# Optimization experiments

Hardware: AMD Instinct MI355X
Metric: run time of the kernel (lower is better)

## Reference

```python
import jax, jax.numpy as jnp
from jax import lax
import numpy as np

WINDOW = 8
ENCOLEN = 128
HID = 128
INT_H = 128


def setup_inputs() -> dict:
    key = jax.random.key(0)
    ks = jax.random.split(key, 16)
    s = 0.05
    B, T = 512, 256
    return {
        "input_X": jax.random.normal(ks[0], (B, T, 7), jnp.float32),
        "W_ih": jax.random.normal(ks[1], (4 * HID, 5), jnp.float32) * s,
        "W_hh": jax.random.normal(ks[2], (4 * HID, HID), jnp.float32) * s,
        "b_ih": jax.random.normal(ks[3], (4 * HID,), jnp.float32) * s,
        "b_hh": jax.random.normal(ks[4], (4 * HID,), jnp.float32) * s,
        "fc1_w": jax.random.normal(ks[5], (HID, HID), jnp.float32) * s,
        "fc1_b": jax.random.normal(ks[6], (HID,), jnp.float32) * s,
        "fc2_w": jax.random.normal(ks[7], (1, HID), jnp.float32) * s,
        "fc2_b": jax.random.normal(ks[8], (1,), jnp.float32) * s,
        "int1_w": jax.random.normal(ks[9], (INT_H, 3), jnp.float32) * s,
        "int1_b": jax.random.normal(ks[10], (INT_H,), jnp.float32) * s,
        "int3_w": jax.random.normal(ks[11], (1, INT_H), jnp.float32) * s,
        "int3_b": jax.random.normal(ks[12], (1,), jnp.float32) * s,
        "scale_w": jax.random.normal(ks[13], (1, 1), jnp.float32) * s,
        "zone_w": jax.random.normal(ks[14], (1, 1), jnp.float32) * s,
    }


def _forward(input_X, W_ih, W_hh, b_ih, b_hh, fc1_w, fc1_b, fc2_w, fc2_b,
             int1_w, int1_b, int3_w, int3_b, scale_w, zone_w):
    B, T, _ = input_X.shape
    w = WINDOW
    T0 = input_X[:, :, 0:1]      # zone temperature
    Ext_X = input_X[:, :, 1:5]   # cols [1,2,3,4]
    Int_X = input_X[:, :, 3:6]   # cols [3,4,5]
    HVAC_X = input_X[:, :, 6:7]  # col [6]

    def lstm_chunk(h, c, xs):  # xs: [B, w, 5]
        def step(carry, x_t):
            h, c = carry
            g = x_t @ W_ih.T + b_ih + h @ W_hh.T + b_hh
            gi, gf, gg, go = jnp.split(g, 4, axis=-1)  # torch gate order i,f,g,o
            c = jax.nn.sigmoid(gf) * c + jax.nn.sigmoid(gi) * jnp.tanh(gg)
            h = jax.nn.sigmoid(go) * jnp.tanh(c)
            return (h, c), None
        (h, c), _ = lax.scan(step, (h, c), jnp.swapaxes(xs, 0, 1))
        return h, c  # final h == lstm_out[:, -1, :]

    def ext_module(h, c, xs):
        h, c = lstm_chunk(h, c, xs)
        o = jax.nn.relu(h @ fc1_w.T + fc1_b)
        return o @ fc2_w.T + fc2_b, h, c  # [B,1]

    # internal module is pointwise per timestep -> vectorize over all T
    # (note: FC2 in the torch module is defined but unused; faithful skip)
    int_all = jax.nn.sigmoid(
        jax.nn.relu(Int_X @ int1_w.T + int1_b) @ int3_w.T + int3_b
    ) @ scale_w.T  # [B,T,1]

    TOut = jnp.zeros((B, T, 1), input_X.dtype).at[:, :w].set(T0[:, :w])
    h = jnp.ones((B, HID), input_X.dtype)
    c = jnp.ones((B, HID), input_X.dtype)
    E = T0[:, w:w + 1, :]  # [B,1,1]

    def enc_step(carry, i):
        TOut, h, c, E = carry
        ratio = i.astype(input_X.dtype) / ENCOLEN
        TOut = lax.dynamic_update_slice(TOut, E, (0, i, 0))
        s = i - w + 1
        Tin = lax.dynamic_slice(T0, (0, s, 0), (B, w, 1))
        TOsl = lax.dynamic_slice(TOut, (0, s, 0), (B, w, 1))
        Exsl = lax.dynamic_slice(Ext_X, (0, s, 0), (B, w, 4))
        embed = jnp.concatenate([Tin * ratio + TOsl * (1.0 - ratio), Exsl], axis=2)
        ext, h, c = ext_module(h, c, embed)
        hv = lax.dynamic_slice(HVAC_X, (0, i, 0), (B, 1, 1))[:, 0]
        it = lax.dynamic_slice(int_all, (0, i, 0), (B, 1, 1))[:, 0]
        total = ext + hv + it  # [B,1]
        T0i = lax.dynamic_slice(T0, (0, i, 0), (B, 1, 1))
        E = ratio * T0i + (1.0 - ratio) * E + (total @ zone_w.T)[:, None, :]
        return (TOut, h, c, E), ext

    (TOut, h, c, E), ext_enc = lax.scan(enc_step, (TOut, h, c, E), jnp.arange(w, ENCOLEN))

    def dec_step(carry, i):
        TOut, h, c, E = carry
        TOut = lax.dynamic_update_slice(TOut, E, (0, i, 0))
        s = i - w + 1
        TOsl = lax.dynamic_slice(TOut, (0, s, 0), (B, w, 1))
        Exsl = lax.dynamic_slice(Ext_X, (0, s, 0), (B, w, 4))
        embed = jnp.concatenate([TOsl, Exsl], axis=2)
        ext, h, c = ext_module(h, c, embed)
        hv = lax.dynamic_slice(HVAC_X, (0, i, 0), (B, 1, 1))[:, 0]
        it = lax.dynamic_slice(int_all, (0, i, 0), (B, 1, 1))[:, 0]
        total = ext + hv + it
        E = (total @ zone_w.T)[:, None, :] + E
        return (TOut, h, c, E), ext

    (TOut, h, c, E), ext_dec = lax.scan(dec_step, (TOut, h, c, E), jnp.arange(ENCOLEN, T))

    Ext_list = jnp.zeros((B, T, 1), input_X.dtype)
    Ext_list = Ext_list.at[:, w:ENCOLEN].set(jnp.swapaxes(ext_enc, 0, 1))
    Ext_list = Ext_list.at[:, ENCOLEN:].set(jnp.swapaxes(ext_dec, 0, 1))
    Int_list = jnp.zeros((B, T, 1), input_X.dtype).at[:, w:].set(int_all[:, w:])
    HVAC_list = HVAC_X  # torch fills HVAC_list with HVAC_X at every step
    return TOut, HVAC_list, (Ext_list, Int_list)


def reference(input_X, W_ih, W_hh, b_ih, b_hh, fc1_w, fc1_b, fc2_w, fc2_b,
              int1_w, int1_b, int3_w, int3_b, scale_w, zone_w):
    return _forward(input_X, W_ih, W_hh, b_ih, b_hh, fc1_w, fc1_b, fc2_w, fc2_b,
                    int1_w, int1_b, int3_w, int3_b, scale_w, zone_w)
```

## Files before the change

### kernel.cpp

```cpp
#include <hip/hip_runtime.h>

#define BT   (512*256)
#define HB0b 192
#define HB1b 320
#define HLENb 448
#define LOG2E 1.44269504088896f

using short8  = __attribute__((ext_vector_type(8))) short;
using floatx4 = __attribute__((ext_vector_type(4))) float;
using int4v   = __attribute__((ext_vector_type(4))) int;
using ushort4v= __attribute__((ext_vector_type(4))) unsigned short;

__device__ inline unsigned short f2bf(float f){
  unsigned int u = __float_as_uint(f);
  u += 0x7FFFu + ((u >> 16) & 1u);
  return (unsigned short)(u >> 16);
}
__device__ inline float bf2f(unsigned short u){
  return __uint_as_float(((unsigned int)u) << 16);
}
__device__ inline float rcpf(float x){ return __builtin_amdgcn_rcpf(x); }
__device__ inline float ex2(float x){ return __builtin_amdgcn_exp2f(x); }

__global__ __launch_bounds__(512,1) void k_seq(
    const float* __restrict__ in,
    const float* __restrict__ Wih,  const float* __restrict__ Whh,
    const float* __restrict__ bih,  const float* __restrict__ bhh,
    const float* __restrict__ fc1w, const float* __restrict__ fc1b,
    const float* __restrict__ fc2w, const float* __restrict__ fc2b,
    const float* __restrict__ i1w,  const float* __restrict__ i1b,
    const float* __restrict__ i3w,  const float* __restrict__ i3b,
    const float* __restrict__ scw,  const float* __restrict__ zonew,
    float* __restrict__ out)
{
  __shared__ __align__(16) signed char hbuf[2][HLENb];
  __shared__ __align__(16) float scratch[640];
  __shared__ __align__(8)  unsigned short toutl[512];
  __shared__ __align__(8)  unsigned short extl[512];
  __shared__ __align__(16) unsigned short exl[2048];
  __shared__ float t0l[512];
  __shared__ float hvitl[512];
  __shared__ __align__(16) float parts[16];

  const int tid = threadIdx.x;
  const int wv  = tid >> 6;
  const int ln  = tid & 63;
  const int l15 = ln & 15;
  const int quad= ln >> 4;
  const int bb  = blockIdx.x;

  {
    int b=tid>>8, tt=tid&255;
    const float* row = in + (2*bb+b)*1792 + tt*7;
    t0l[tid] = row[0];
    exl[tid*4+0]=f2bf(row[1]); exl[tid*4+1]=f2bf(row[2]);
    exl[tid*4+2]=f2bf(row[3]); exl[tid*4+3]=f2bf(row[4]);
  }
  for(int p=tid; p<2*HLENb; p+=512) ((signed char*)hbuf)[p]=0;
  if(tid<16) toutl[(tid>>3)*256+(tid&7)] = f2bf(in[(2*bb+(tid>>3))*1792+(tid&7)*7]);
  float* lw4 = scratch;
  float* l3  = scratch + 512;
  if(tid<128){
    lw4[tid*4+0]=i1w[tid*3+0]; lw4[tid*4+1]=i1w[tid*3+1];
    lw4[tid*4+2]=i1w[tid*3+2]; lw4[tid*4+3]=i1b[tid];
    l3[tid]=i3w[tid];
  }
  __syncthreads();
  if(tid<256) hbuf[0][((tid>>7)? HB1b:HB0b) + (tid&127)] = 127;

  {
    const float b30=i3b[0], sc0=scw[0];
    int b=tid>>8, t=tid&255;
    const float* row = in + (2*bb+b)*1792 + t*7;
    float x0=row[3],x1=row[4],x2=row[5], acc=0.f;
    #pragma unroll 8
    for(int j=0;j<128;j++){
      float r=fmaxf(lw4[j*4]*x0+lw4[j*4+1]*x1+lw4[j*4+2]*x2+lw4[j*4+3],0.f);
      acc += r*l3[j];
    }
    float v = rcpf(1.f+__expf(-(acc+b30)))*sc0;
    float itv = (t<8)?0.f:v;
    int gb = 2*bb+b;
    hvitl[tid] = row[6] + itv;
    out[3*BT+gb*256+t]=itv;
    out[BT+gb*256+t]=row[6];
    if(t<8){ out[gb*256+t]=row[0]; out[2*BT+gb*256+t]=0.f; }
  }

  int4v wq[4][2];
  float dq[4];
  short8 xfr[4];
  float  bsum[4];
  #pragma unroll
  for(int g=0;g<4;g++){
    int n = 128*g + 16*wv + l15;
    bsum[g] = (bih[n]+bhh[n])*LOG2E;
    const float* wr = Whh + n*128;
    float mx = 1e-20f;
    for(int j=0;j<128;j++) mx = fmaxf(mx, fabsf(wr[j]));
    float qs = 127.f/mx;
    dq[g] = mx * (LOG2E/16129.f);
    #pragma unroll
    for(int c=0;c<2;c++){
      int4v v4;
      #pragma unroll
      for(int d=0;d<4;d++){
        int pk=0;
        #pragma unroll
        for(int bq=0;bq<4;bq++){
          int kk = c*64 + quad*16 + d*4 + bq;
          int q = __float2int_rn(wr[kk]*qs);
          pk |= (q & 255) << (8*bq);
        }
        v4[d]=pk;
      }
      wq[g][c]=v4;
    }
    short8 f;
    #pragma unroll
    for(int j=0;j<8;j++){ int kk=quad*8+j; f[j]=(short)f2bf(kk<5?Wih[n*5+kk]*LOG2E:0.f); }
    xfr[g]=f;
  }
  int4v fq[2]; float dqf;
  {
    int n2 = 16*wv + l15;
    const float* fr = fc1w + n2*128;
    float mx = 1e-20f;
    for(int j=0;j<128;j++) mx = fmaxf(mx, fabsf(fr[j]));
    float qs = 127.f/mx;
    dqf = mx * (1.f/16129.f);
    #pragma unroll
    for(int c=0;c<2;c++){
      int4v v4;
      #pragma unroll
      for(int d=0;d<4;d++){
        int pk=0;
        #pragma unroll
        for(int bq=0;bq<4;bq++){
          int kk = c*64 + quad*16 + d*4 + bq;
          int q = __float2int_rn(fr[kk]*qs);
          pk |= (q & 255) << (8*bq);
        }
        v4[d]=pk;
      }
      fq[c]=v4;
    }
  }

  const int  u     = 16*wv + l15;
  const int  bm    = quad & 1;
  const int  arow  = ((l15&3)==0) ? (((l15>>2)&1)? HB1b : HB0b) : 0;
  const int  aoff  = arow + quad*16;
  const int  hwoff = (bm? HB1b:HB0b) + u;
  const int  bpa0  = ((quad&1)<<7) | (l15<<2);
  const int  bpa1  = bpa0 + 64;
  const float fb    = fc1b[u];
  const float fcw_u = fc2w[u];
  const float fc2b0 = fc2b[0];
  const float zwv   = zonew[0];
  const floatx4 ZV  = {0.f,0.f,0.f,0.f};
  const int4v   ZI  = {0,0,0,0};
  const short8  Z8  = 0;
  float E0 = in[(2*bb)*1792 + 56];
  float E1 = in[(2*bb+1)*1792 + 56];
  float c0 = 1.f;
  __syncthreads();

  #pragma unroll 1
  for(int i=8;i<256;i++){
    if(i>8){
      floatx4 pa=*(const floatx4*)&parts[0];
      floatx4 pb=*(const floatx4*)&parts[4];
      floatx4 pc=*(const floatx4*)&parts[8];
      floatx4 pd=*(const floatx4*)&parts[12];
      float ext0=((pa[0]+pa[1])+(pa[2]+pa[3]))+((pb[0]+pb[1])+(pb[2]+pb[3]))+fc2b0;
      float ext1=((pc[0]+pc[1])+(pc[2]+pc[3]))+((pd[0]+pd[1])+(pd[2]+pd[3]))+fc2b0;
      int ip = i-1;
      float tot0 = ext0 + hvitl[ip];
      float tot1 = ext1 + hvitl[256+ip];
      if(ip<128){
        float ratio=(float)ip*0.0078125f;
        E0 = ratio*t0l[ip]     + (1.f-ratio)*E0 + tot0*zwv;
        E1 = ratio*t0l[256+ip] + (1.f-ratio)*E1 + tot1*zwv;
      } else {
        E0 += tot0*zwv;
        E1 += tot1*zwv;
      }
      if(tid==0){ extl[ip]=f2bf(ext0); extl[256+ip]=f2bf(ext1); }
    }
    if(tid==0){ toutl[i]=f2bf(E0); toutl[256+i]=f2bf(E1); }
    float xv[8][4];
    {
      short8 ea = Z8;
      if(quad==0){
        int bE=l15>>3, kk=l15&7, p=i-7+kk;
        float tos = (p==i) ? (bE? E1:E0) : bf2f(toutl[bE*256+p]);
        float tmix;
        if(i<128){
          float ratio=(float)i*0.0078125f;
          tmix = t0l[bE*256+p]*ratio + tos*(1.f-ratio);
        } else tmix = tos;
        ea[0]=(short)f2bf(tmix);
        ushort4v e4 = *(const ushort4v*)&exl[(bE*256+p)*4];
        ea[1]=(short)e4[0]; ea[2]=(short)e4[1];
        ea[3]=(short)e4[2]; ea[4]=(short)e4[3];
      }
      #pragma unroll
      for(int g=0;g<4;g++){
        floatx4 z=__builtin_amdgcn_mfma_f32_16x16x32_bf16(ea, xfr[g], ZV,0,0,0);
        #pragma unroll
        for(int r=0;r<4;r++){
          int zi = __float_as_int(z[r]+bsum[g]);
          xv[r][g]   = __int_as_float(__builtin_amdgcn_ds_bpermute(bpa0, zi));
          xv[r+4][g] = __int_as_float(__builtin_amdgcn_ds_bpermute(bpa1, zi));
        }
      }
    }

    #pragma unroll
    for(int k=0;k<8;k++){
      const signed char* hb = &hbuf[k&1][0];
      int4v a0 = *(const int4v*)(hb + aoff);
      int4v a1 = *(const int4v*)(hb + aoff + 64);
      int4v acc[4];
      #pragma unroll
      for(int g=0;g<4;g++){
        int4v z = __builtin_amdgcn_mfma_i32_16x16x64_i8(a0, wq[g][0], ZI,0,0,0);
        z = __builtin_amdgcn_mfma_i32_16x16x64_i8(a1, wq[g][1], z,0,0,0);
        acc[g]=z;
      }
      float gi=fmaf((float)acc[0][0],dq[0],xv[k][0]);
      float gf=fmaf((float)acc[1][0],dq[1],xv[k][1]);
      float gg=fmaf((float)acc[2][0],dq[2],xv[k][2]);
      float go=fmaf((float)acc[3][0],dq[3],xv[k][3]);
      float ef =ex2(-gf);
      float egi=ex2(-gi);
      float egg=ex2(-2.f*gg);
      float sf = rcpf(1.f+ef);
      float itn=(1.f-egg)*rcpf((1.f+egi)*(1.f+egg));
      c0 = sf*c0 + itn;
      float ego=ex2(-go);
      float ec =ex2(-2.8853900818f*c0);
      float hv2=(1.f-ec)*rcpf((1.f+ego)*(1.f+ec));
      int q = __float2int_rn(hv2*127.f);
      hbuf[(k+1)&1][hwoff] = (signed char)q;
      __syncthreads();
    }

    {
      const signed char* hb = &hbuf[0][0];
      int4v a0 = *(const int4v*)(hb + aoff);
      int4v a1 = *(const int4v*)(hb + aoff + 64);
      int4v z = __builtin_amdgcn_mfma_i32_16x16x64_i8(a0, fq[0], ZI,0,0,0);
      z = __builtin_amdgcn_mfma_i32_16x16x64_i8(a1, fq[1], z,0,0,0);
      float fv = (float)z[0]*dqf + fb;
      float pv = fmaxf(fv,0.f)*fcw_u;
      pv += __shfl_xor(pv, 1, 64);
      pv += __shfl_xor(pv, 2, 64);
      pv += __shfl_xor(pv, 4, 64);
      pv += __shfl_xor(pv, 8, 64);
      if(ln==0)       parts[wv]   = pv;
      else if(ln==16) parts[8+wv] = pv;
    }
    __syncthreads();
  }

  if(tid==0){
    float ext0 = ((parts[0]+parts[1])+(parts[2]+parts[3]))
               + ((parts[4]+parts[5])+(parts[6]+parts[7])) + fc2b0;
    float ext1 = ((parts[8]+parts[9])+(parts[10]+parts[11]))
               + ((parts[12]+parts[13])+(parts[14]+parts[15])) + fc2b0;
    extl[255]=f2bf(ext0); extl[511]=f2bf(ext1);
  }
  __syncthreads();

  for(int p=tid; p<496; p+=512){
    int b = (p>=248) ? 1 : 0;
    int i2 = p - b*248 + 8;
    int gb = 2*bb + b;
    out[gb*256+i2]      = bf2f(toutl[b*256+i2]);
    out[2*BT+gb*256+i2] = bf2f(extl[b*256+i2]);
  }
}

extern "C" void kernel_launch(void* const* d_in, const int* in_sizes, int n_in,
                              void* d_out, int out_size, void* d_ws, size_t ws_size,
                              hipStream_t stream)
{
  const float* in   = (const float*)d_in[0];
  const float* Wih  = (const float*)d_in[1];
  const float* Whh  = (const float*)d_in[2];
  const float* bih  = (const float*)d_in[3];
  const float* bhh  = (const float*)d_in[4];
  const float* fc1w = (const float*)d_in[5];
  const float* fc1b = (const float*)d_in[6];
  const float* fc2w = (const float*)d_in[7];
  const float* fc2b = (const float*)d_in[8];
  const float* i1w  = (const float*)d_in[9];
  const float* i1b  = (const float*)d_in[10];
  const float* i3w  = (const float*)d_in[11];
  const float* i3b  = (const float*)d_in[12];
  const float* scw  = (const float*)d_in[13];
  const float* zw   = (const float*)d_in[14];
  float* out = (float*)d_out;

  k_seq<<<dim3(256), dim3(512), 0, stream>>>(in, Wih, Whh, bih, bhh,
                                             fc1w, fc1b, fc2w, fc2b,
                                             i1w, i1b, i3w, i3b, scw, zw, out);
}
```

Baseline: 969.3 us.

## Process one batch row per block and launch twice as many blocks

```diff
diff --git a/kernel.cpp b/kernel.cpp
--- a/kernel.cpp
+++ b/kernel.cpp
@@ -2,8 +2,7 @@
 
 #define BT   (512*256)
 #define HB0b 192
-#define HB1b 320
-#define HLENb 448
+#define HLENb 320
 #define LOG2E 1.44269504088896f
 
 using short8  = __attribute__((ext_vector_type(8))) short;
@@ -22,7 +21,7 @@
 __device__ inline float rcpf(float x){ return __builtin_amdgcn_rcpf(x); }
 __device__ inline float ex2(float x){ return __builtin_amdgcn_exp2f(x); }
 
-__global__ __launch_bounds__(512,1) void k_seq(
+__global__ __launch_bounds__(512,2) void k_seq(
     const float* __restrict__ in,
     const float* __restrict__ Wih,  const float* __restrict__ Whh,
     const float* __restrict__ bih,  const float* __restrict__ bhh,
@@ -35,12 +34,12 @@
 {
   __shared__ __align__(16) signed char hbuf[2][HLENb];
   __shared__ __align__(16) float scratch[640];
-  __shared__ __align__(8)  unsigned short toutl[512];
-  __shared__ __align__(8)  unsigned short extl[512];
-  __shared__ __align__(16) unsigned short exl[2048];
-  __shared__ float t0l[512];
-  __shared__ float hvitl[512];
-  __shared__ __align__(16) float parts[16];
+  __shared__ __align__(8)  unsigned short toutl[256];
+  __shared__ __align__(8)  unsigned short extl[256];
+  __shared__ __align__(16) unsigned short exl[1024];
+  __shared__ float t0l[256];
+  __shared__ float hvitl[256];
+  __shared__ __align__(16) float parts[8];
 
   const int tid = threadIdx.x;
   const int wv  = tid >> 6;
@@ -49,29 +48,29 @@
   const int quad= ln >> 4;
   const int bb  = blockIdx.x;
 
-  {
-    int b=tid>>8, tt=tid&255;
-    const float* row = in + (2*bb+b)*1792 + tt*7;
+  if(tid<256){
+    const float* row = in + bb*1792 + tid*7;
     t0l[tid] = row[0];
     exl[tid*4+0]=f2bf(row[1]); exl[tid*4+1]=f2bf(row[2]);
     exl[tid*4+2]=f2bf(row[3]); exl[tid*4+3]=f2bf(row[4]);
   }
   for(int p=tid; p<2*HLENb; p+=512) ((signed char*)hbuf)[p]=0;
-  if(tid<16) toutl[(tid>>3)*256+(tid&7)] = f2bf(in[(2*bb+(tid>>3))*1792+(tid&7)*7]);
+  if(tid<8) toutl[tid] = f2bf(in[bb*1792+tid*7]);
   float* lw4 = scratch;
   float* l3  = scratch + 512;
-  if(tid<128){
-    lw4[tid*4+0]=i1w[tid*3+0]; lw4[tid*4+1]=i1w[tid*3+1];
-    lw4[tid*4+2]=i1w[tid*3+2]; lw4[tid*4+3]=i1b[tid];
-    l3[tid]=i3w[tid];
+  if(tid>=256 && tid<384){
+    int j=tid-256;
+    lw4[j*4+0]=i1w[j*3+0]; lw4[j*4+1]=i1w[j*3+1];
+    lw4[j*4+2]=i1w[j*3+2]; lw4[j*4+3]=i1b[j];
+    l3[j]=i3w[j];
   }
   __syncthreads();
-  if(tid<256) hbuf[0][((tid>>7)? HB1b:HB0b) + (tid&127)] = 127;
-
-  {
+  if(tid<128) hbuf[0][HB0b+tid] = 127;
+
+  if(tid<256){
     const float b30=i3b[0], sc0=scw[0];
-    int b=tid>>8, t=tid&255;
-    const float* row = in + (2*bb+b)*1792 + t*7;
+    int t=tid;
+    const float* row = in + bb*1792 + t*7;
     float x0=row[3],x1=row[4],x2=row[5], acc=0.f;
     #pragma unroll 8
     for(int j=0;j<128;j++){
@@ -80,11 +79,10 @@
     }
     float v = rcpf(1.f+__expf(-(acc+b30)))*sc0;
     float itv = (t<8)?0.f:v;
-    int gb = 2*bb+b;
-    hvitl[tid] = row[6] + itv;
-    out[3*BT+gb*256+t]=itv;
-    out[BT+gb*256+t]=row[6];
-    if(t<8){ out[gb*256+t]=row[0]; out[2*BT+gb*256+t]=0.f; }
+    hvitl[t] = row[6] + itv;
+    out[3*BT+bb*256+t]=itv;
+    out[BT+bb*256+t]=row[6];
+    if(t<8){ out[bb*256+t]=row[0]; out[2*BT+bb*256+t]=0.f; }
   }
 
   int4v wq[4][2];
@@ -148,11 +146,10 @@
   }
 
   const int  u     = 16*wv + l15;
-  const int  bm    = quad & 1;
-  const int  arow  = ((l15&3)==0) ? (((l15>>2)&1)? HB1b : HB0b) : 0;
+  const int  arow  = ((l15&3)==0) ? HB0b : 0;
   const int  aoff  = arow + quad*16;
-  const int  hwoff = (bm? HB1b:HB0b) + u;
-  const int  bpa0  = ((quad&1)<<7) | (l15<<2);
+  const int  hwoff = HB0b + u;
+  const int  bpa0  = l15<<2;
   const int  bpa1  = bpa0 + 64;
   const float fb    = fc1b[u];
   const float fcw_u = fc2w[u];
@@ -161,8 +158,7 @@
   const floatx4 ZV  = {0.f,0.f,0.f,0.f};
   const int4v   ZI  = {0,0,0,0};
   const short8  Z8  = 0;
-  float E0 = in[(2*bb)*1792 + 56];
-  float E1 = in[(2*bb+1)*1792 + 56];
+  float E0 = in[bb*1792 + 56];
   float c0 = 1.f;
   __syncthreads();
 
@@ -171,37 +167,31 @@
     if(i>8){
       floatx4 pa=*(const floatx4*)&parts[0];
       floatx4 pb=*(const floatx4*)&parts[4];
-      floatx4 pc=*(const floatx4*)&parts[8];
-      floatx4 pd=*(const floatx4*)&parts[12];
       float ext0=((pa[0]+pa[1])+(pa[2]+pa[3]))+((pb[0]+pb[1])+(pb[2]+pb[3]))+fc2b0;
-      float ext1=((pc[0]+pc[1])+(pc[2]+pc[3]))+((pd[0]+pd[1])+(pd[2]+pd[3]))+fc2b0;
       int ip = i-1;
       float tot0 = ext0 + hvitl[ip];
-      float tot1 = ext1 + hvitl[256+ip];
       if(ip<128){
         float ratio=(float)ip*0.0078125f;
-        E0 = ratio*t0l[ip]     + (1.f-ratio)*E0 + tot0*zwv;
-        E1 = ratio*t0l[256+ip] + (1.f-ratio)*E1 + tot1*zwv;
+        E0 = ratio*t0l[ip] + (1.f-ratio)*E0 + tot0*zwv;
       } else {
         E0 += tot0*zwv;
-        E1 += tot1*zwv;
-      }
-      if(tid==0){ extl[ip]=f2bf(ext0); extl[256+ip]=f2bf(ext1); }
-    }
-    if(tid==0){ toutl[i]=f2bf(E0); toutl[256+i]=f2bf(E1); }
+      }
+      if(tid==0) extl[ip]=f2bf(ext0);
+    }
+    if(tid==0) toutl[i]=f2bf(E0);
     float xv[8][4];
     {
       short8 ea = Z8;
-      if(quad==0){
-        int bE=l15>>3, kk=l15&7, p=i-7+kk;
-        float tos = (p==i) ? (bE? E1:E0) : bf2f(toutl[bE*256+p]);
+      if(ln<8){
+        int p=i-7+ln;
+        float tos = (p==i) ? E0 : bf2f(toutl[p]);
         float tmix;
         if(i<128){
           float ratio=(float)i*0.0078125f;
-          tmix = t0l[bE*256+p]*ratio + tos*(1.f-ratio);
+          tmix = t0l[p]*ratio + tos*(1.f-ratio);
         } else tmix = tos;
         ea[0]=(short)f2bf(tmix);
-        ushort4v e4 = *(const ushort4v*)&exl[(bE*256+p)*4];
+        ushort4v e4 = *(const ushort4v*)&exl[p*4];
         ea[1]=(short)e4[0]; ea[2]=(short)e4[1];
         ea[3]=(short)e4[2]; ea[4]=(short)e4[3];
       }
@@ -259,8 +249,7 @@
       pv += __shfl_xor(pv, 2, 64);
       pv += __shfl_xor(pv, 4, 64);
       pv += __shfl_xor(pv, 8, 64);
-      if(ln==0)       parts[wv]   = pv;
-      else if(ln==16) parts[8+wv] = pv;
+      if(ln==0) parts[wv] = pv;
     }
     __syncthreads();
   }
@@ -268,18 +257,14 @@
   if(tid==0){
     float ext0 = ((parts[0]+parts[1])+(parts[2]+parts[3]))
                + ((parts[4]+parts[5])+(parts[6]+parts[7])) + fc2b0;
-    float ext1 = ((parts[8]+parts[9])+(parts[10]+parts[11]))
-               + ((parts[12]+parts[13])+(parts[14]+parts[15])) + fc2b0;
-    extl[255]=f2bf(ext0); extl[511]=f2bf(ext1);
+    extl[255]=f2bf(ext0);
   }
   __syncthreads();
 
-  for(int p=tid; p<496; p+=512){
-    int b = (p>=248) ? 1 : 0;
-    int i2 = p - b*248 + 8;
-    int gb = 2*bb + b;
-    out[gb*256+i2]      = bf2f(toutl[b*256+i2]);
-    out[2*BT+gb*256+i2] = bf2f(extl[b*256+i2]);
+  if(tid<248){
+    int i2 = tid + 8;
+    out[bb*256+i2]      = bf2f(toutl[i2]);
+    out[2*BT+bb*256+i2] = bf2f(extl[i2]);
   }
 }
 
@@ -304,7 +289,7 @@
   const float* zw   = (const float*)d_in[14];
   float* out = (float*)d_out;
 
-  k_seq<<<dim3(256), dim3(512), 0, stream>>>(in, Wih, Whh, bih, bhh,
+  k_seq<<<dim3(512), dim3(512), 0, stream>>>(in, Wih, Whh, bih, bhh,
                                              fc1w, fc1b, fc2w, fc2b,
                                              i1w, i1b, i3w, i3b, scw, zw, out);
 }
```

Result: slower. 1.774 ms (+83.1%).

## Precompute next window's input projection during current step and split MFMA accumulation chains

Applied to the files above, without the earlier changes.

```diff
diff --git a/kernel.cpp b/kernel.cpp
--- a/kernel.cpp
+++ b/kernel.cpp
@@ -91,10 +91,12 @@
   float dq[4];
   short8 xfr[4];
   float  bsum[4];
+  float  wihc[4];
   #pragma unroll
   for(int g=0;g<4;g++){
     int n = 128*g + 16*wv + l15;
     bsum[g] = (bih[n]+bhh[n])*LOG2E;
+    wihc[g] = Wih[n*5]*LOG2E;
     const float* wr = Whh + n*128;
     float mx = 1e-20f;
     for(int j=0;j<128;j++) mx = fmaxf(mx, fabsf(wr[j]));
@@ -165,6 +167,49 @@
   float E1 = in[(2*bb+1)*1792 + 56];
   float c0 = 1.f;
   __syncthreads();
+
+  float xv[8][4];
+  float xvn[8][4];
+
+  auto bulk = [&](int it, bool exact7, float (&dst)[8][4]) {
+    short8 ea = Z8;
+    if(quad==0){
+      int bE=l15>>3, kk=l15&7, p=it-7+kk;
+      bool lt = (it<128);
+      float ratio=(float)it*0.0078125f;
+      float tmix;
+      if(kk==7){
+        if(exact7){
+          float tos = bE? E1:E0;
+          tmix = lt ? t0l[bE*256+it]*ratio + tos*(1.f-ratio) : tos;
+        } else {
+          tmix = lt ? t0l[bE*256+it]*ratio : 0.f;
+        }
+      } else if(kk==6){
+        float tos = exact7 ? bf2f(toutl[bE*256+p]) : (bE? E1:E0);
+        tmix = lt ? t0l[bE*256+p]*ratio + tos*(1.f-ratio) : tos;
+      } else {
+        float tos = bf2f(toutl[bE*256+p]);
+        tmix = lt ? t0l[bE*256+p]*ratio + tos*(1.f-ratio) : tos;
+      }
+      ea[0]=(short)f2bf(tmix);
+      ushort4v e4 = *(const ushort4v*)&exl[(bE*256+p)*4];
+      ea[1]=(short)e4[0]; ea[2]=(short)e4[1];
+      ea[3]=(short)e4[2]; ea[4]=(short)e4[3];
+    }
+    #pragma unroll
+    for(int g=0;g<4;g++){
+      floatx4 z=__builtin_amdgcn_mfma_f32_16x16x32_bf16(ea, xfr[g], ZV,0,0,0);
+      #pragma unroll
+      for(int r=0;r<4;r++){
+        int zi = __float_as_int(z[r]+bsum[g]);
+        dst[r][g]   = __int_as_float(__builtin_amdgcn_ds_bpermute(bpa0, zi));
+        dst[r+4][g] = __int_as_float(__builtin_amdgcn_ds_bpermute(bpa1, zi));
+      }
+    }
+  };
+
+  bulk(8, true, xv);
 
   #pragma unroll 1
   for(int i=8;i<256;i++){
@@ -187,52 +232,39 @@
         E1 += tot1*zwv;
       }
       if(tid==0){ extl[ip]=f2bf(ext0); extl[256+ip]=f2bf(ext1); }
+      float kap = (i<128) ? (1.f-(float)i*0.0078125f) : 1.f;
+      float ce  = kap * (bm ? E1 : E0);
+      #pragma unroll
+      for(int k2=0;k2<7;k2++)
+        #pragma unroll
+        for(int g=0;g<4;g++) xv[k2][g]=xvn[k2][g];
+      #pragma unroll
+      for(int g=0;g<4;g++) xv[7][g] = fmaf(ce, wihc[g], xvn[7][g]);
     }
     if(tid==0){ toutl[i]=f2bf(E0); toutl[256+i]=f2bf(E1); }
-    float xv[8][4];
-    {
-      short8 ea = Z8;
-      if(quad==0){
-        int bE=l15>>3, kk=l15&7, p=i-7+kk;
-        float tos = (p==i) ? (bE? E1:E0) : bf2f(toutl[bE*256+p]);
-        float tmix;
-        if(i<128){
-          float ratio=(float)i*0.0078125f;
-          tmix = t0l[bE*256+p]*ratio + tos*(1.f-ratio);
-        } else tmix = tos;
-        ea[0]=(short)f2bf(tmix);
-        ushort4v e4 = *(const ushort4v*)&exl[(bE*256+p)*4];
-        ea[1]=(short)e4[0]; ea[2]=(short)e4[1];
-        ea[3]=(short)e4[2]; ea[4]=(short)e4[3];
-      }
-      #pragma unroll
-      for(int g=0;g<4;g++){
-        floatx4 z=__builtin_amdgcn_mfma_f32_16x16x32_bf16(ea, xfr[g], ZV,0,0,0);
-        #pragma unroll
-        for(int r=0;r<4;r++){
-          int zi = __float_as_int(z[r]+bsum[g]);
-          xv[r][g]   = __int_as_float(__builtin_amdgcn_ds_bpermute(bpa0, zi));
-          xv[r+4][g] = __int_as_float(__builtin_amdgcn_ds_bpermute(bpa1, zi));
-        }
-      }
-    }
+
+    int4v a0h = *(const int4v*)(&hbuf[0][0] + aoff);
+    int4v a1h = *(const int4v*)(&hbuf[0][0] + aoff + 64);
+
+    if(i<255) bulk(i+1, false, xvn);
 
     #pragma unroll
     for(int k=0;k<8;k++){
       const signed char* hb = &hbuf[k&1][0];
-      int4v a0 = *(const int4v*)(hb + aoff);
-      int4v a1 = *(const int4v*)(hb + aoff + 64);
-      int4v acc[4];
+      int4v a0, a1;
+      if(k==0){ a0=a0h; a1=a1h; }
+      else { a0 = *(const int4v*)(hb + aoff); a1 = *(const int4v*)(hb + aoff + 64); }
+      int accs[4];
       #pragma unroll
       for(int g=0;g<4;g++){
-        int4v z = __builtin_amdgcn_mfma_i32_16x16x64_i8(a0, wq[g][0], ZI,0,0,0);
-        z = __builtin_amdgcn_mfma_i32_16x16x64_i8(a1, wq[g][1], z,0,0,0);
-        acc[g]=z;
-      }
-      float gi=fmaf((float)acc[0][0],dq[0],xv[k][0]);
-      float gf=fmaf((float)acc[1][0],dq[1],xv[k][1]);
-      float gg=fmaf((float)acc[2][0],dq[2],xv[k][2]);
-      float go=fmaf((float)acc[3][0],dq[3],xv[k][3]);
+        int4v za = __builtin_amdgcn_mfma_i32_16x16x64_i8(a0, wq[g][0], ZI,0,0,0);
+        int4v zb = __builtin_amdgcn_mfma_i32_16x16x64_i8(a1, wq[g][1], ZI,0,0,0);
+        accs[g] = za[0]+zb[0];
+      }
+      float gi=fmaf((float)accs[0],dq[0],xv[k][0]);
+      float gf=fmaf((float)accs[1],dq[1],xv[k][1]);
+      float gg=fmaf((float)accs[2],dq[2],xv[k][2]);
+      float go=fmaf((float)accs[3],dq[3],xv[k][3]);
       float ef =ex2(-gf);
       float egi=ex2(-gi);
       float egg=ex2(-2.f*gg);
@@ -251,9 +283,9 @@
       const signed char* hb = &hbuf[0][0];
       int4v a0 = *(const int4v*)(hb + aoff);
       int4v a1 = *(const int4v*)(hb + aoff + 64);
-      int4v z = __builtin_amdgcn_mfma_i32_16x16x64_i8(a0, fq[0], ZI,0,0,0);
-      z = __builtin_amdgcn_mfma_i32_16x16x64_i8(a1, fq[1], z,0,0,0);
-      float fv = (float)z[0]*dqf + fb;
+      int4v za = __builtin_amdgcn_mfma_i32_16x16x64_i8(a0, fq[0], ZI,0,0,0);
+      int4v zb = __builtin_amdgcn_mfma_i32_16x16x64_i8(a1, fq[1], ZI,0,0,0);
+      float fv = (float)(za[0]+zb[0])*dqf + fb;
       float pv = fmaxf(fv,0.f)*fcw_u;
       pv += __shfl_xor(pv, 1, 64);
       pv += __shfl_xor(pv, 2, 64);
```

Result: slower. 1.109 ms (+14.4%).

## Pack input projections as bf16 pairs and break MFMA accumulate chains

Applied to the files above, without the earlier changes.

```diff
diff --git a/kernel.cpp b/kernel.cpp
--- a/kernel.cpp
+++ b/kernel.cpp
@@ -2,8 +2,8 @@
 
 #define BT   (512*256)
 #define HB0b 192
-#define HB1b 320
-#define HLENb 448
+#define HB1b 336
+#define HLENb 464
 #define LOG2E 1.44269504088896f
 
 using short8  = __attribute__((ext_vector_type(8))) short;
@@ -189,7 +189,7 @@
       if(tid==0){ extl[ip]=f2bf(ext0); extl[256+ip]=f2bf(ext1); }
     }
     if(tid==0){ toutl[i]=f2bf(E0); toutl[256+i]=f2bf(E1); }
-    float xv[8][4];
+    int xvp[8][2];
     {
       short8 ea = Z8;
       if(quad==0){
@@ -206,13 +206,17 @@
         ea[3]=(short)e4[2]; ea[4]=(short)e4[3];
       }
       #pragma unroll
-      for(int g=0;g<4;g++){
-        floatx4 z=__builtin_amdgcn_mfma_f32_16x16x32_bf16(ea, xfr[g], ZV,0,0,0);
+      for(int gp=0; gp<2; gp++){
+        floatx4 zl=__builtin_amdgcn_mfma_f32_16x16x32_bf16(ea, xfr[2*gp],   ZV,0,0,0);
+        floatx4 zh=__builtin_amdgcn_mfma_f32_16x16x32_bf16(ea, xfr[2*gp+1], ZV,0,0,0);
         #pragma unroll
         for(int r=0;r<4;r++){
-          int zi = __float_as_int(z[r]+bsum[g]);
-          xv[r][g]   = __int_as_float(__builtin_amdgcn_ds_bpermute(bpa0, zi));
-          xv[r+4][g] = __int_as_float(__builtin_amdgcn_ds_bpermute(bpa1, zi));
+          float lo = zl[r]+bsum[2*gp];
+          float hi = zh[r]+bsum[2*gp+1];
+          int pk;
+          asm("v_cvt_pk_bf16_f32 %0, %1, %2" : "=v"(pk) : "v"(lo), "v"(hi));
+          xvp[r][gp]   = __builtin_amdgcn_ds_bpermute(bpa0, pk);
+          xvp[r+4][gp] = __builtin_amdgcn_ds_bpermute(bpa1, pk);
         }
       }
     }
@@ -222,17 +226,22 @@
       const signed char* hb = &hbuf[k&1][0];
       int4v a0 = *(const int4v*)(hb + aoff);
       int4v a1 = *(const int4v*)(hb + aoff + 64);
-      int4v acc[4];
+      int accs[4];
       #pragma unroll
       for(int g=0;g<4;g++){
-        int4v z = __builtin_amdgcn_mfma_i32_16x16x64_i8(a0, wq[g][0], ZI,0,0,0);
-        z = __builtin_amdgcn_mfma_i32_16x16x64_i8(a1, wq[g][1], z,0,0,0);
-        acc[g]=z;
-      }
-      float gi=fmaf((float)acc[0][0],dq[0],xv[k][0]);
-      float gf=fmaf((float)acc[1][0],dq[1],xv[k][1]);
-      float gg=fmaf((float)acc[2][0],dq[2],xv[k][2]);
-      float go=fmaf((float)acc[3][0],dq[3],xv[k][3]);
+        int4v za = __builtin_amdgcn_mfma_i32_16x16x64_i8(a0, wq[g][0], ZI,0,0,0);
+        int4v zb = __builtin_amdgcn_mfma_i32_16x16x64_i8(a1, wq[g][1], ZI,0,0,0);
+        accs[g] = za[0]+zb[0];
+      }
+      int p0=xvp[k][0], p1=xvp[k][1];
+      float xi = __uint_as_float(((unsigned)p0)<<16);
+      float xf = __uint_as_float((unsigned)p0 & 0xffff0000u);
+      float xgg= __uint_as_float(((unsigned)p1)<<16);
+      float xo = __uint_as_float((unsigned)p1 & 0xffff0000u);
+      float gi=fmaf((float)accs[0],dq[0],xi);
+      float gf=fmaf((float)accs[1],dq[1],xf);
+      float gg=fmaf((float)accs[2],dq[2],xgg);
+      float go=fmaf((float)accs[3],dq[3],xo);
       float ef =ex2(-gf);
       float egi=ex2(-gi);
       float egg=ex2(-2.f*gg);
@@ -243,7 +252,7 @@
       float ec =ex2(-2.8853900818f*c0);
       float hv2=(1.f-ec)*rcpf((1.f+ego)*(1.f+ec));
       int q = __float2int_rn(hv2*127.f);
-      hbuf[(k+1)&1][hwoff] = (signed char)q;
+      if(ln<32) hbuf[(k+1)&1][hwoff] = (signed char)q;
       __syncthreads();
     }
 
@@ -251,9 +260,9 @@
       const signed char* hb = &hbuf[0][0];
       int4v a0 = *(const int4v*)(hb + aoff);
       int4v a1 = *(const int4v*)(hb + aoff + 64);
-      int4v z = __builtin_amdgcn_mfma_i32_16x16x64_i8(a0, fq[0], ZI,0,0,0);
-      z = __builtin_amdgcn_mfma_i32_16x16x64_i8(a1, fq[1], z,0,0,0);
-      float fv = (float)z[0]*dqf + fb;
+      int4v za = __builtin_amdgcn_mfma_i32_16x16x64_i8(a0, fq[0], ZI,0,0,0);
+      int4v zb = __builtin_amdgcn_mfma_i32_16x16x64_i8(a1, fq[1], ZI,0,0,0);
+      float fv = (float)(za[0]+zb[0])*dqf + fb;
       float pv = fmaxf(fv,0.f)*fcw_u;
       pv += __shfl_xor(pv, 1, 64);
       pv += __shfl_xor(pv, 2, 64);
```

After: 1.048 ms. 1.08x slower.
